# Performance work log

Measured on AMD Instinct MI355X. Metric: run time of the kernel, lower is better.

## Reference

```python
import jax, jax.numpy as jnp
import numpy as np

DIM = 512
NUM_HEADS = 8
HEAD_DIM = DIM // NUM_HEADS
SCALE = HEAD_DIM ** -0.5
HIDDEN = int(DIM * 4.0)
LN_EPS = 1e-5


def layer_norm(x, w, b):
    mu = jnp.mean(x, axis=-1, keepdims=True)
    var = jnp.var(x, axis=-1, keepdims=True)
    return (x - mu) * jax.lax.rsqrt(var + LN_EPS) * w + b


def setup_inputs() -> dict:
    key = jax.random.key(0)
    ks = jax.random.split(key, 8)
    s = 0.02
    return {
        "x": jax.random.normal(ks[0], (8, 4096, DIM), dtype=jnp.float32),
        "ln1_w": jnp.ones((DIM,), jnp.float32),
        "ln1_b": jnp.zeros((DIM,), jnp.float32),
        "qkv_w": jax.random.normal(ks[1], (3 * DIM, DIM), jnp.float32) * s,
        "proj_w": jax.random.normal(ks[2], (DIM, DIM), jnp.float32) * s,
        "proj_b": jnp.zeros((DIM,), jnp.float32),
        "ln2_w": jnp.ones((DIM,), jnp.float32),
        "ln2_b": jnp.zeros((DIM,), jnp.float32),
        "fc1_w": jax.random.normal(ks[3], (HIDDEN, DIM), jnp.float32) * s,
        "fc1_b": jnp.zeros((HIDDEN,), jnp.float32),
        "fc2_w": jax.random.normal(ks[4], (DIM, HIDDEN), jnp.float32) * s,
        "fc2_b": jnp.zeros((DIM,), jnp.float32),
        "eca_w": jax.random.normal(ks[5], (1, 1, 3), jnp.float32) * 0.5,
    }


def channel_attention(x, qkv_w, proj_w, proj_b):
    B, N, C = x.shape
    qkv = (x @ qkv_w.T).reshape(B, N, 3, NUM_HEADS, HEAD_DIM)
    qkv = qkv.transpose(2, 0, 3, 1, 4)  # (3, B, h, N, hd)
    q, k, v = qkv[0], qkv[1] * SCALE, qkv[2]
    # cross-covariance attention: (hd x hd) per head
    attn = jax.nn.softmax(jnp.einsum("bhnd,bhne->bhde", k, v), axis=-1)
    out = jnp.einsum("bhde,bhne->bhnd", attn, q)  # (B, h, N, hd)
    out = out.transpose(0, 2, 1, 3).reshape(B, N, C)
    return out @ proj_w.T + proj_b


def mlp_eca(x, fc1_w, fc1_b, fc2_w, fc2_b, eca_w):
    B, N, C = x.shape
    H = W = int(np.sqrt(N))
    h = jax.nn.gelu(x @ fc1_w.T + fc1_b, approximate=False)
    y = h @ fc2_w.T + fc2_b  # (B, N, C)
    # faithful replication of torch .view(B, C, H, W) on contiguous (B, N, C)
    y4 = y.reshape(B, C, H, W)
    pooled = jnp.mean(y4, axis=(2, 3))  # (B, C)
    conv = jax.lax.conv_general_dilated(
        pooled[:, None, :], eca_w, window_strides=(1,), padding=[(1, 1)],
        dimension_numbers=("NCW", "OIW", "NCW"))[:, 0, :]  # (B, C)
    gate = jax.nn.sigmoid(conv)[:, :, None, None]
    y4 = y4 * gate + y4
    return y4.reshape(B, C, H * W).transpose(0, 2, 1)  # (B, N, C)


def reference(x, ln1_w, ln1_b, qkv_w, proj_w, proj_b, ln2_w, ln2_b,
              fc1_w, fc1_b, fc2_w, fc2_b, eca_w):
    cur = layer_norm(x, ln1_w, ln1_b)
    x = x + channel_attention(cur, qkv_w, proj_w, proj_b)
    x = x + mlp_eca(layer_norm(x, ln2_w, ln2_b), fc1_w, fc1_b, fc2_w, fc2_b, eca_w)
    return x
```

## Files before the change

### kernel.cpp

```cpp
#include <hip/hip_runtime.h>
#include <hip/hip_bf16.h>

typedef __bf16 bf16;
typedef __bf16 bf16x8 __attribute__((ext_vector_type(8)));
typedef float floatx4 __attribute__((ext_vector_type(4)));

#define B_    8
#define N_    4096
#define C_    512
#define BN_   32768
#define HID_  2048
#define SCALE_ 0.125f

__device__ __forceinline__ void load_lds16(const void* g, void* l) {
    __builtin_amdgcn_global_load_lds(
        (const __attribute__((address_space(1))) void*)g,
        (__attribute__((address_space(3))) void*)l, 16, 0, 0);
}

__device__ __forceinline__ float gelu_fast(float v) {
    float c = fmaf(v * v, 0.044715f, 1.0f) * v;
    float e = __builtin_amdgcn_exp2f(-2.3022082f * c);
    return v * __builtin_amdgcn_rcpf(1.0f + e);
}

__global__ void sniff_kernel(const unsigned int* __restrict__ xw, int* __restrict__ flag)
{
    int t = threadIdx.x;
    int votes = 0;
#pragma unroll
    for (int i = 0; i < 4; i++) {
        unsigned w = xw[t * 4 + i];
        if (w == 0u) continue;
        unsigned a = w & 0xFFFFu;
        unsigned e = (a >> 7) & 0xFFu;
        if (a != 0u && e >= 110u && e <= 135u) votes++; else votes--;
    }
#pragma unroll
    for (int off = 32; off; off >>= 1) votes += __shfl_xor(votes, off);
    __shared__ int s[4];
    if ((t & 63) == 0) s[t >> 6] = votes;
    __syncthreads();
    if (t == 0) *flag = (s[0] + s[1] + s[2] + s[3]) > 0 ? 1 : 0;
}

struct ConvArgs {
    const void* src[12];
    unsigned    dstoff[12];
    int         n[12];
};

__global__ __launch_bounds__(256) void convert_params(
    ConvArgs args, char* __restrict__ ws, const int* __restrict__ flag)
{
    int seg = blockIdx.y;
    int n = args.n[seg];
    int base = blockIdx.x * 2048;
    if (base >= n) return;
    bf16* dst = (bf16*)(ws + args.dstoff[seg]);
    const void* src = args.src[seg];
    bool isbf = (*flag != 0);
#pragma unroll
    for (int j = 0; j < 8; j++) {
        int idx = base + threadIdx.x + j * 256;
        if (idx < n) {
            float v = isbf ? (float)((const bf16*)src)[idx]
                           : ((const float*)src)[idx];
            dst[idx] = (bf16)v;
        }
    }
}

__device__ __forceinline__ void ln_core(float f[8], const bf16* w, const bf16* b,
                                        int lane, bf16* outp)
{
    float s = 0.f, sq = 0.f;
#pragma unroll
    for (int j = 0; j < 8; j++) { s += f[j]; sq += f[j]*f[j]; }
#pragma unroll
    for (int off = 32; off; off >>= 1) { s += __shfl_xor(s, off); sq += __shfl_xor(sq, off); }
    float mean = s * (1.f/512.f);
    float var  = sq * (1.f/512.f) - mean*mean;
    float inv  = rsqrtf(var + 1e-5f);
    bf16x8 wv = *(const bf16x8*)(w + lane*8);
    bf16x8 bv = *(const bf16x8*)(b + lane*8);
    bf16x8 o;
#pragma unroll
    for (int j = 0; j < 8; j++) o[j] = (bf16)((f[j]-mean)*inv*(float)wv[j] + (float)bv[j]);
    *(bf16x8*)outp = o;
}

__global__ __launch_bounds__(256) void ln_dyn_kernel(
    const void* __restrict__ xv, const bf16* __restrict__ w,
    const bf16* __restrict__ b, bf16* __restrict__ out, const int* __restrict__ flag)
{
    int wave = threadIdx.x >> 6, lane = threadIdx.x & 63;
    size_t row = (size_t)blockIdx.x * 4 + wave;
    float f[8];
    if (*flag) {
        bf16x8 v = *(const bf16x8*)((const bf16*)xv + row * C_ + lane * 8);
#pragma unroll
        for (int j = 0; j < 8; j++) f[j] = (float)v[j];
    } else {
        const float4* p = (const float4*)((const float*)xv + row * C_ + lane * 8);
        float4 v0 = p[0], v1 = p[1];
        f[0]=v0.x; f[1]=v0.y; f[2]=v0.z; f[3]=v0.w;
        f[4]=v1.x; f[5]=v1.y; f[6]=v1.z; f[7]=v1.w;
    }
    ln_core(f, w, b, lane, out + row * C_ + lane*8);
}

__global__ __launch_bounds__(256) void ln_b16_kernel(
    const bf16* __restrict__ x, const bf16* __restrict__ w,
    const bf16* __restrict__ b, bf16* __restrict__ out)
{
    int wave = threadIdx.x >> 6, lane = threadIdx.x & 63;
    size_t row = (size_t)blockIdx.x * 4 + wave;
    bf16x8 v = *(const bf16x8*)(x + row * C_ + lane * 8);
    float f[8];
#pragma unroll
    for (int j = 0; j < 8; j++) f[j] = (float)v[j];
    ln_core(f, w, b, lane, out + row * C_ + lane*8);
}

__global__ __launch_bounds__(256) void ln_f32_kernel(
    const float* __restrict__ x, const bf16* __restrict__ w,
    const bf16* __restrict__ b, bf16* __restrict__ out)
{
    int wave = threadIdx.x >> 6, lane = threadIdx.x & 63;
    size_t row = (size_t)blockIdx.x * 4 + wave;
    const float4* p = (const float4*)(x + row * C_ + lane * 8);
    float4 v0 = p[0], v1 = p[1];
    float f[8] = { v0.x, v0.y, v0.z, v0.w, v1.x, v1.y, v1.z, v1.w };
    ln_core(f, w, b, lane, out + row * C_ + lane*8);
}

enum { EPI_NONE = 0, EPI_BIAS = 1, EPI_BIAS_RESID = 2, EPI_BIAS_GELU = 3, EPI_QKV = 4 };

#define RD_A(dst, S, H)                                                        \
    _Pragma("unroll") for (int mi = 0; mi < 4; mi++) {                         \
        int row = wm * 64 + mi * 16 + l16;                                     \
        _Pragma("unroll") for (int ks = 0; ks < 2; ks++)                       \
            dst[mi][ks] = *(const bf16x8*)(&Asl[S][H][0][0] + row * 64 +       \
                ((ks * 32 + quad * 8) ^ ((row & 7) << 3)));                    \
    }
#define RD_B(dst, S, H)                                                        \
    _Pragma("unroll") for (int ni = 0; ni < 2; ni++) {                         \
        int row = wn * 32 + ni * 16 + l16;                                     \
        _Pragma("unroll") for (int ks = 0; ks < 2; ks++)                       \
            dst[ni][ks] = *(const bf16x8*)(&Bsl[S][H][0][0] + row * 64 +       \
                ((ks * 32 + quad * 8) ^ ((row & 7) << 3)));                    \
    }
#define MM(AF, BF, AH, BH)                                                     \
    __builtin_amdgcn_s_setprio(1);                                             \
    _Pragma("unroll") for (int mi = 0; mi < 4; mi++)                           \
    _Pragma("unroll") for (int ni = 0; ni < 2; ni++)                           \
    _Pragma("unroll") for (int ks = 0; ks < 2; ks++)                           \
        acc[(AH)*4+mi][(BH)*2+ni] = __builtin_amdgcn_mfma_f32_16x16x32_bf16(   \
            AF[mi][ks], BF[ni][ks], acc[(AH)*4+mi][(BH)*2+ni], 0, 0, 0);       \
    __builtin_amdgcn_s_setprio(0);
#define STAGE2(GB, LB)                                                         \
    { load_lds16((GB) + goff0, (LB) + loff0);                                  \
      load_lds16((GB) + goff1, (LB) + loff1); }

template<typename OutT, int EPI>
__global__ __launch_bounds__(512, 2) void gemm256(
    const bf16* __restrict__ A, const bf16* __restrict__ W,
    const bf16* __restrict__ bias, const void* __restrict__ resid,
    const int* __restrict__ flag,
    OutT* __restrict__ Cout, bf16* __restrict__ Cout2, int M, int Nn, int K)
{
    __shared__ bf16 Asl[2][2][128][64];
    __shared__ bf16 Bsl[2][2][128][64];
    const int t = threadIdx.x;
    const int wv = t >> 6, lane = t & 63;
    const int quad = lane >> 4, l16 = lane & 15;
    const int wm = wv >> 2, wn = wv & 3;
    const int Nt = Nn >> 8;
    const int total = (M >> 8) * Nt;
    const int G = gridDim.x;
    const int NKT = K >> 6;

    const int c0 = t, c1 = 512 + t;
    const int r0 = c0 >> 3, r1 = c1 >> 3;
    const size_t goff0 = (size_t)r0 * K + (size_t)(((c0 & 7) ^ (r0 & 7)) * 8);
    const size_t goff1 = (size_t)r1 * K + (size_t)(((c1 & 7) ^ (r1 & 7)) * 8);
    const int loff0 = c0 * 8, loff1 = c1 * 8;

    int id = blockIdx.x;
    if (id >= total) return;
    int m0 = (((id >> 3) / Nt) * 8 + (id & 7)) * 256;
    int n0 = ((id >> 3) % Nt) * 256;

    STAGE2(A + (size_t)m0 * K,         &Asl[0][0][0][0]);
    STAGE2(W + (size_t)n0 * K,         &Bsl[0][0][0][0]);
    STAGE2(A + (size_t)(m0 + 128) * K, &Asl[0][1][0][0]);
    STAGE2(W + (size_t)n0 * K + 64,    &Bsl[1][0][0][0]);
    STAGE2(W + (size_t)(n0 + 128) * K, &Bsl[0][1][0][0]);
    STAGE2(A + (size_t)m0 * K + 64,    &Asl[1][0][0][0]);
    asm volatile("s_waitcnt vmcnt(4)");
    __builtin_amdgcn_s_barrier();

    bf16x8 afE[4][2], afO[4][2], bf0[2][2], bf1[2][2];
    RD_A(afE, 0, 0)

    for (;;) {
        const int idn = id + G;
        const bool hn = idn < total;
        int m0n = 0, n0n = 0;
        if (hn) {
            m0n = (((idn >> 3) / Nt) * 8 + (idn & 7)) * 256;
            n0n = ((idn >> 3) % Nt) * 256;
        }

        floatx4 acc[8][4] = {};

        for (int kt = 0; kt < NKT; ++kt) {
            const int s = kt & 1;
            {
                const bf16* p = (kt + 1 < NKT)
                    ? A + (size_t)(m0 + 128) * K + (size_t)(kt + 1) * 64
                    : (hn ? A + (size_t)(m0n + 128) * K : nullptr);
                if (p) STAGE2(p, &Asl[s ^ 1][1][0][0]);
            }
            __builtin_amdgcn_s_barrier();
            RD_B(bf0, s, 0)
            RD_B(bf1, s, 1)
            __builtin_amdgcn_sched_barrier(0);
            MM(afE, bf0, 0, 0)
            {
                const bf16* p = (kt + 1 < NKT)
                    ? W + (size_t)(n0 + 128) * K + (size_t)(kt + 1) * 64
                    : (hn ? W + (size_t)(n0n + 128) * K : nullptr);
                if (p) STAGE2(p, &Bsl[s ^ 1][1][0][0]);
            }
            __builtin_amdgcn_s_barrier();
            RD_A(afO, s, 1)
            __builtin_amdgcn_sched_barrier(0);
            MM(afE, bf1, 0, 1)
            {
                const bf16* p = (kt + 2 < NKT)
                    ? A + (size_t)m0 * K + (size_t)(kt + 2) * 64
                    : (hn ? A + (size_t)m0n * K + (size_t)(kt + 2 - NKT) * 64 : nullptr);
                if (p) STAGE2(p, &Asl[s][0][0][0]);
            }
            __builtin_amdgcn_s_barrier();
            MM(afO, bf1, 1, 1)
            {
                const bf16* p = (kt + 2 < NKT)
                    ? W + (size_t)n0 * K + (size_t)(kt + 2) * 64
                    : (hn ? W + (size_t)n0n * K + (size_t)(kt + 2 - NKT) * 64 : nullptr);
                if (p) STAGE2(p, &Bsl[s][0][0][0]);
            }
            if (kt + 1 < NKT || hn) {
                if (kt + 2 < NKT || hn) asm volatile("s_waitcnt vmcnt(4)");
                else                    asm volatile("s_waitcnt vmcnt(0)");
            }
            __builtin_amdgcn_s_barrier();
            if (kt + 1 < NKT || hn) { RD_A(afE, s ^ 1, 0) }
            __builtin_amdgcn_sched_barrier(0);
            MM(afO, bf0, 1, 0)
        }

        size_t ldc = (size_t)Nn; int csub = 0; bool to2 = false;
        if (EPI == EPI_QKV) {
            if (n0 >= 512) { to2 = true; ldc = 1024; csub = 512; }
            else           { ldc = 512; }
        }
        bool isbf = false;
        if (EPI == EPI_BIAS_RESID) isbf = (*flag != 0);

#pragma unroll
        for (int mg = 0; mg < 8; mg++) {
            int rowg = m0 + (mg >> 2) * 128 + wm * 64 + (mg & 3) * 16 + quad * 4;
#pragma unroll
            for (int ng = 0; ng < 4; ng++) {
                int col = n0 + (ng >> 1) * 128 + wn * 32 + (ng & 1) * 16 + l16;
                float bv = (EPI == EPI_BIAS || EPI == EPI_BIAS_RESID || EPI == EPI_BIAS_GELU)
                           ? (float)bias[col] : 0.f;
#pragma unroll
                for (int r = 0; r < 4; r++) {
                    size_t idx = (size_t)(rowg + r) * ldc + (col - csub);
                    float v = acc[mg][ng][r] + bv;
                    if (EPI == EPI_BIAS_RESID) {
                        float rres = isbf ? (float)((const bf16*)resid)[idx]
                                          : ((const float*)resid)[idx];
                        v += rres;
                    }
                    if (EPI == EPI_BIAS_GELU)  v = gelu_fast(v);
                    if (EPI == EPI_QKV && to2) Cout2[idx] = (bf16)v;
                    else                       Cout[idx]  = (OutT)v;
                }
            }
        }

        if (!hn) break;
        id = idn; m0 = m0n; n0 = n0n;
    }
}

__global__ __launch_bounds__(256) void attn_logits_mfma(
    const bf16* __restrict__ kv, float* __restrict__ partial)
{
    __shared__ bf16 Kt[64][136];
    __shared__ bf16 Vt[64][136];
    int s = blockIdx.x, bh = blockIdx.y, b = bh >> 3, h = bh & 7;
    int t = threadIdx.x, wave = t >> 6, lane = t & 63;
    int quad = lane >> 4, l16 = lane & 15;
    floatx4 acc[4] = {};
    for (int c = 0; c < 4; c++) {
        int n0 = s * 512 + c * 128;
        {
            int isv = t >> 7;
            int r   = t & 127;
            const bf16* gp = &kv[((size_t)b * N_ + n0 + r) * 1024 + h * 64 + isv * 512];
            bf16x8 rowv[8];
#pragma unroll
            for (int u = 0; u < 8; u++) rowv[u] = *(const bf16x8*)(gp + u * 8);
            bf16 (*dst)[136] = isv ? Vt : Kt;
#pragma unroll
            for (int u = 0; u < 8; u++)
#pragma unroll
                for (int jj = 0; jj < 8; jj++)
                    dst[u * 8 + jj][r] = rowv[u][jj];
        }
        __syncthreads();
#pragma unroll
        for (int ks = 0; ks < 4; ks++) {
            bf16x8 af = *(const bf16x8*)&Kt[wave * 16 + l16][ks * 32 + quad * 8];
#pragma unroll
            for (int ni = 0; ni < 4; ni++) {
                bf16x8 bfv = *(const bf16x8*)&Vt[ni * 16 + l16][ks * 32 + quad * 8];
                acc[ni] = __builtin_amdgcn_mfma_f32_16x16x32_bf16(af, bfv, acc[ni], 0, 0, 0);
            }
        }
        __syncthreads();
    }
    float* p = partial + ((size_t)bh * 8 + s) * 4096;
#pragma unroll
    for (int ni = 0; ni < 4; ni++)
#pragma unroll
        for (int r = 0; r < 4; r++)
            p[(wave * 16 + quad * 4 + r) * 64 + ni * 16 + l16] = acc[ni][r];
}

__global__ __launch_bounds__(256) void attn_softmax_kernel(
    const float* __restrict__ partial, bf16* __restrict__ attnb)
{
    int bh = blockIdx.y;
    int wave = threadIdx.x >> 6, lane = threadIdx.x & 63;
    for (int r = 0; r < 4; r++) {
        int d = blockIdx.x * 16 + wave * 4 + r;
        float v = 0.f;
#pragma unroll
        for (int s = 0; s < 8; s++) v += partial[((size_t)bh*8 + s)*4096 + d*64 + lane];
        v *= SCALE_;
        float m = v;
#pragma unroll
        for (int off = 32; off; off >>= 1) m = fmaxf(m, __shfl_xor(m, off));
        float p = expf(v - m);
        float sum = p;
#pragma unroll
        for (int off = 32; off; off >>= 1) sum += __shfl_xor(sum, off);
        attnb[(size_t)bh*4096 + d*64 + lane] = (bf16)(p / sum);
    }
}

__global__ __launch_bounds__(256) void attn_apply_mfma(
    const bf16* __restrict__ q, const bf16* __restrict__ attnb,
    bf16* __restrict__ outT)
{
    int bh = blockIdx.y, b = bh >> 3, h = bh & 7;
    int t = threadIdx.x, wave = t >> 6, lane = t & 63;
    int quad = lane >> 4, l16 = lane & 15;
    int nbase = blockIdx.x * 256 + wave * 64;
    bf16x8 bfrag[4][2];
#pragma unroll
    for (int di = 0; di < 4; di++)
#pragma unroll
        for (int ks = 0; ks < 2; ks++)
            bfrag[di][ks] = *(const bf16x8*)&attnb[(size_t)bh*4096 + (di*16 + l16)*64 + ks*32 + quad*8];
    floatx4 acc[4][4] = {};
#pragma unroll
    for (int mi = 0; mi < 4; mi++) {
#pragma unroll
        for (int ks = 0; ks < 2; ks++) {
            bf16x8 af = *(const bf16x8*)&q[((size_t)b*N_ + nbase + mi*16 + l16)*512 + h*64 + ks*32 + quad*8];
#pragma unroll
            for (int di = 0; di < 4; di++)
                acc[mi][di] = __builtin_amdgcn_mfma_f32_16x16x32_bf16(af, bfrag[di][ks], acc[mi][di], 0, 0, 0);
        }
    }
#pragma unroll
    for (int mi = 0; mi < 4; mi++)
#pragma unroll
        for (int di = 0; di < 4; di++)
#pragma unroll
            for (int r = 0; r < 4; r++)
                outT[((size_t)b*N_ + nbase + mi*16 + quad*4 + r)*512 + h*64 + di*16 + l16] =
                    (bf16)acc[mi][di][r];
}

__global__ __launch_bounds__(256) void pooled_kernel(
    const bf16* __restrict__ y, float* __restrict__ pooled)
{
    int bc = blockIdx.x;
    const bf16* p = y + (size_t)bc * 4096 + threadIdx.x * 16;
    float s = 0.f;
#pragma unroll
    for (int i = 0; i < 2; i++) {
        bf16x8 v = *(const bf16x8*)(p + i*8);
#pragma unroll
        for (int j = 0; j < 8; j++) s += (float)v[j];
    }
#pragma unroll
    for (int off = 32; off; off >>= 1) s += __shfl_xor(s, off);
    __shared__ float red[4];
    if ((threadIdx.x & 63) == 0) red[threadIdx.x >> 6] = s;
    __syncthreads();
    if (threadIdx.x == 0)
        pooled[bc] = (red[0] + red[1] + red[2] + red[3]) * (1.f/4096.f);
}

__global__ void gate_kernel(const float* __restrict__ pooled,
                            const bf16* __restrict__ eca_w, float* __restrict__ gate1)
{
    int c = threadIdx.x, b = blockIdx.x;
    float w0 = (float)eca_w[0], w1 = (float)eca_w[1], w2 = (float)eca_w[2];
    const float* p = pooled + b * 512;
    float conv = w1 * p[c];
    if (c > 0)   conv += w0 * p[c-1];
    if (c < 511) conv += w2 * p[c+1];
    float g = 1.f / (1.f + expf(-conv));
    gate1[b * 512 + c] = 1.f + g;
}

__global__ __launch_bounds__(256) void final_rmw(
    const bf16* __restrict__ y, const float* __restrict__ gate1,
    float* __restrict__ out)
{
    int b = blockIdx.z, c0 = blockIdx.y * 64, n0 = blockIdx.x * 64;
    __shared__ float ytile[64][65];
    int t = threadIdx.x;
#pragma unroll
    for (int i = 0; i < 2; i++) {
        int chunk = t * 2 + i;
        int ci = chunk >> 3, nj = (chunk & 7) * 8;
        bf16x8 v = *(const bf16x8*)&y[(size_t)b * ((size_t)N_*C_) + (size_t)(c0+ci) * 4096 + n0 + nj];
#pragma unroll
        for (int j = 0; j < 8; j++) ytile[ci][nj+j] = (float)v[j];
    }
    __syncthreads();
    int cc = t & 63, nb = t >> 6;
    float g = gate1[b * 512 + c0 + cc];
    for (int p = 0; p < 16; p++) {
        int nr = p * 4 + nb;
        size_t idx = ((size_t)b * N_ + n0 + nr) * C_ + c0 + cc;
        out[idx] = out[idx] + g * ytile[cc][nr];
    }
}

__global__ __launch_bounds__(256) void final_fresh(
    const bf16* __restrict__ y, const bf16* __restrict__ x2b,
    const float* __restrict__ gate1, float* __restrict__ out)
{
    int b = blockIdx.z, c0 = blockIdx.y * 64, n0 = blockIdx.x * 64;
    __shared__ float ytile[64][65];
    int t = threadIdx.x;
#pragma unroll
    for (int i = 0; i < 2; i++) {
        int chunk = t * 2 + i;
        int ci = chunk >> 3, nj = (chunk & 7) * 8;
        bf16x8 v = *(const bf16x8*)&y[(size_t)b * ((size_t)N_*C_) + (size_t)(c0+ci) * 4096 + n0 + nj];
#pragma unroll
        for (int j = 0; j < 8; j++) ytile[ci][nj+j] = (float)v[j];
    }
    __syncthreads();
    int cc = t & 63, nb = t >> 6;
    float g = gate1[b * 512 + c0 + cc];
    for (int p = 0; p < 16; p++) {
        int nr = p * 4 + nb;
        size_t idx = ((size_t)b * N_ + n0 + nr) * C_ + c0 + cc;
        out[idx] = (float)x2b[idx] + g * ytile[cc][nr];
    }
}

extern "C" void kernel_launch(void* const* d_in, const int* in_sizes, int n_in,
                              void* d_out, int out_size, void* d_ws, size_t ws_size,
                              hipStream_t stream)
{
    float* outf = (float*)d_out;
    bf16*  outb = (bf16*)d_out;
    char* ws = (char*)d_ws;

    int*   flag    = (int*)ws;
    float* pooled  = (float*)(ws + 4096);
    float* gate1   = (float*)(ws + 20480);
    bf16* ln1_w = (bf16*)(ws + 65536);
    bf16* ln1_b = (bf16*)(ws + 67584);
    bf16* ln2_w = (bf16*)(ws + 69632);
    bf16* ln2_b = (bf16*)(ws + 71680);
    bf16* proj_b= (bf16*)(ws + 73728);
    bf16* fc2_b = (bf16*)(ws + 75776);
    bf16* eca_w = (bf16*)(ws + 77824);
    bf16* fc1_b = (bf16*)(ws + 81920);
    bf16* qkv_w = (bf16*)(ws + ((size_t)1 << 20));
    bf16* proj_w= (bf16*)(ws + (size_t)2621440);
    bf16* fc1_w = (bf16*)(ws + ((size_t)3 << 20));
    bf16* fc2_w = (bf16*)(ws + ((size_t)5 << 20));
    float* partial = (float*)(ws + ((size_t)7  << 20));
    bf16*  attnb   = (bf16*)(ws + ((size_t)15 << 20));
    bf16*  T1      = (bf16*)(ws + ((size_t)16 << 20));
    bf16*  kvbuf   = (bf16*)(ws + ((size_t)48 << 20));
    bf16*  hbuf    = kvbuf;
    bf16*  x2b     = (bf16*)(ws + ((size_t)176 << 20));

    const bool fat = ws_size >= ((size_t)212 << 20);

    sniff_kernel<<<1, 256, 0, stream>>>((const unsigned int*)d_in[0], flag);

    ConvArgs ca;
    const int   srcidx[12] = { 1, 2, 6, 7, 5, 11, 12, 9, 3, 4, 8, 10 };
    const unsigned offs[12] = { 65536, 67584, 69632, 71680, 73728, 75776, 77824, 81920,
                                1u<<20, 2621440u, 3u<<20, 5u<<20 };
    for (int i = 0; i < 12; i++) {
        ca.src[i] = d_in[srcidx[i]];
        ca.dstoff[i] = offs[i];
        ca.n[i] = in_sizes[srcidx[i]];
    }
    convert_params<<<dim3(512, 12), 256, 0, stream>>>(ca, ws, flag);

    ln_dyn_kernel<<<BN_/4, 256, 0, stream>>>(d_in[0], ln1_w, ln1_b, T1, flag);

    gemm256<bf16, EPI_QKV><<<256, 512, 0, stream>>>(
        T1, qkv_w, nullptr, nullptr, flag, outb, kvbuf, BN_, 1536, 512);

    attn_logits_mfma<<<dim3(8, 64), 256, 0, stream>>>(kvbuf, partial);
    attn_softmax_kernel<<<dim3(4, 64), 256, 0, stream>>>(partial, attnb);
    attn_apply_mfma<<<dim3(16, 64), 256, 0, stream>>>(outb, attnb, T1);

    if (fat) {
        gemm256<bf16, EPI_BIAS_RESID><<<256, 512, 0, stream>>>(
            T1, proj_w, proj_b, d_in[0], flag, x2b, nullptr, BN_, 512, 512);
        ln_b16_kernel<<<BN_/4, 256, 0, stream>>>(x2b, ln2_w, ln2_b, T1);
        gemm256<bf16, EPI_BIAS_GELU><<<256, 512, 0, stream>>>(
            T1, fc1_w, fc1_b, nullptr, flag, hbuf, nullptr, BN_, 2048, 512);
        gemm256<bf16, EPI_BIAS><<<256, 512, 0, stream>>>(
            hbuf, fc2_w, fc2_b, nullptr, flag, T1, nullptr, BN_, 512, 2048);
        pooled_kernel<<<4096, 256, 0, stream>>>(T1, pooled);
        gate_kernel<<<8, 512, 0, stream>>>(pooled, eca_w, gate1);
        final_fresh<<<dim3(64, 8, 8), 256, 0, stream>>>(T1, x2b, gate1, outf);
    } else {
        gemm256<float, EPI_BIAS_RESID><<<256, 512, 0, stream>>>(
            T1, proj_w, proj_b, d_in[0], flag, outf, nullptr, BN_, 512, 512);
        ln_f32_kernel<<<BN_/4, 256, 0, stream>>>(outf, ln2_w, ln2_b, T1);
        for (int ch = 0; ch < 2; ch++) {
            bf16* Tch = T1 + (size_t)ch * 16384 * 512;
            gemm256<bf16, EPI_BIAS_GELU><<<256, 512, 0, stream>>>(
                Tch, fc1_w, fc1_b, nullptr, flag, hbuf, nullptr, 16384, 2048, 512);
            gemm256<bf16, EPI_BIAS><<<128, 512, 0, stream>>>(
                hbuf, fc2_w, fc2_b, nullptr, flag, Tch, nullptr, 16384, 512, 2048);
        }
        pooled_kernel<<<4096, 256, 0, stream>>>(T1, pooled);
        gate_kernel<<<8, 512, 0, stream>>>(pooled, eca_w, gate1);
        final_rmw<<<dim3(64, 8, 8), 256, 0, stream>>>(T1, gate1, outf);
    }
}
```

Baseline: 538.1 us.

## Unroll GEMM k-loop by two with precomputed LDS fragment pointers

Restructures the inner loop of the 256x256 bf16 GEMM into a two-stage unrolled KTILE macro, so the LDS double-buffer stage index is a compile-time constant. Swizzled LDS read addresses are precomputed once into pointer arrays instead of being recomputed on every read. The A-fragment prefetch across iterations is replaced by a single fragment buffer refilled inside each phase, with an explicit lgkmcnt(0) wait before each MFMA group. The prologue load order is also changed so the second half of the W tile is resident before the first barrier. This aims to cut address arithmetic and register pressure, but it gives up some overlap of LDS reads with MFMA work.

Result: faster. 521.9 us (-3.0%).

```diff
diff --git a/kernel.cpp b/kernel.cpp
--- a/kernel.cpp
+++ b/kernel.cpp
@@ -137,20 +137,6 @@
 
 enum { EPI_NONE = 0, EPI_BIAS = 1, EPI_BIAS_RESID = 2, EPI_BIAS_GELU = 3, EPI_QKV = 4 };
 
-#define RD_A(dst, S, H)                                                        \
-    _Pragma("unroll") for (int mi = 0; mi < 4; mi++) {                         \
-        int row = wm * 64 + mi * 16 + l16;                                     \
-        _Pragma("unroll") for (int ks = 0; ks < 2; ks++)                       \
-            dst[mi][ks] = *(const bf16x8*)(&Asl[S][H][0][0] + row * 64 +       \
-                ((ks * 32 + quad * 8) ^ ((row & 7) << 3)));                    \
-    }
-#define RD_B(dst, S, H)                                                        \
-    _Pragma("unroll") for (int ni = 0; ni < 2; ni++) {                         \
-        int row = wn * 32 + ni * 16 + l16;                                     \
-        _Pragma("unroll") for (int ks = 0; ks < 2; ks++)                       \
-            dst[ni][ks] = *(const bf16x8*)(&Bsl[S][H][0][0] + row * 64 +       \
-                ((ks * 32 + quad * 8) ^ ((row & 7) << 3)));                    \
-    }
 #define MM(AF, BF, AH, BH)                                                     \
     __builtin_amdgcn_s_setprio(1);                                             \
     _Pragma("unroll") for (int mi = 0; mi < 4; mi++)                           \
@@ -163,6 +149,63 @@
     { load_lds16((GB) + goff0, (LB) + loff0);                                  \
       load_lds16((GB) + goff1, (LB) + loff1); }
 
+#define KTILE(KT, S)                                                           \
+{                                                                              \
+    bf16x8 af[4][2], bf0[2][2], bf1[2][2];                                     \
+                         \
+    _Pragma("unroll") for (int mi = 0; mi < 4; mi++)                           \
+    _Pragma("unroll") for (int ks = 0; ks < 2; ks++)                           \
+        af[mi][ks] = *(const bf16x8*)(pa[mi][ks] + (S) * 16384);               \
+    _Pragma("unroll") for (int ni = 0; ni < 2; ni++)                           \
+    _Pragma("unroll") for (int ks = 0; ks < 2; ks++)                           \
+        bf0[ni][ks] = *(const bf16x8*)(pb[ni][ks] + (S) * 16384);              \
+    { const bf16* sp = ((KT) + 1 < NKT)                                        \
+          ? A + (size_t)(m0 + 128) * K + (size_t)((KT) + 1) * 64               \
+          : (hn ? A + (size_t)(m0n + 128) * K : nullptr);                      \
+      if (sp) STAGE2(sp, &Asl[(S) ^ 1][1][0][0]); }                            \
+    __builtin_amdgcn_s_barrier();                                              \
+    asm volatile("s_waitcnt lgkmcnt(0)");                                      \
+    __builtin_amdgcn_sched_barrier(0);                                         \
+    MM(af, bf0, 0, 0)                                                          \
+                             \
+    _Pragma("unroll") for (int ni = 0; ni < 2; ni++)                           \
+    _Pragma("unroll") for (int ks = 0; ks < 2; ks++)                           \
+        bf1[ni][ks] = *(const bf16x8*)(pb[ni][ks] + (S) * 16384 + 8192);       \
+    { const bf16* sp = ((KT) + 1 < NKT)                                        \
+          ? W + (size_t)(n0 + 128) * K + (size_t)((KT) + 1) * 64               \
+          : (hn ? W + (size_t)(n0n + 128) * K : nullptr);                      \
+      if (sp) STAGE2(sp, &Bsl[(S) ^ 1][1][0][0]); }                            \
+    __builtin_amdgcn_s_barrier();                                              \
+    asm volatile("s_waitcnt lgkmcnt(0)");                                      \
+    __builtin_amdgcn_sched_barrier(0);                                         \
+    MM(af, bf1, 0, 1)                                                          \
+                            \
+    _Pragma("unroll") for (int mi = 0; mi < 4; mi++)                           \
+    _Pragma("unroll") for (int ks = 0; ks < 2; ks++)                           \
+        af[mi][ks] = *(const bf16x8*)(pa[mi][ks] + (S) * 16384 + 8192);        \
+    { const bf16* sp = ((KT) + 2 < NKT)                                        \
+          ? A + (size_t)m0 * K + (size_t)((KT) + 2) * 64                       \
+          : (hn ? A + (size_t)m0n * K + (size_t)((KT) + 2 - NKT) * 64          \
+               : nullptr);                                                     \
+      if (sp) STAGE2(sp, &Asl[(S)][0][0][0]); }                                \
+    __builtin_amdgcn_s_barrier();                                              \
+    asm volatile("s_waitcnt lgkmcnt(0)");                                      \
+    __builtin_amdgcn_sched_barrier(0);                                         \
+    MM(af, bf1, 1, 1)                                                          \
+               \
+    { const bf16* sp = ((KT) + 2 < NKT)                                        \
+          ? W + (size_t)n0 * K + (size_t)((KT) + 2) * 64                       \
+          : (hn ? W + (size_t)n0n * K + (size_t)((KT) + 2 - NKT) * 64          \
+               : nullptr);                                                     \
+      if (sp) STAGE2(sp, &Bsl[(S)][0][0][0]); }                                \
+    if ((KT) + 1 < NKT || hn) {                                                \
+        if ((KT) + 2 < NKT || hn) asm volatile("s_waitcnt vmcnt(4)");          \
+        else                      asm volatile("s_waitcnt vmcnt(0)");          \
+    }                                                                          \
+    __builtin_amdgcn_s_barrier();                                              \
+    MM(af, bf0, 1, 0)                                                          \
+}
+
 template<typename OutT, int EPI>
 __global__ __launch_bounds__(512, 2) void gemm256(
     const bf16* __restrict__ A, const bf16* __restrict__ W,
@@ -181,6 +224,25 @@
     const int G = gridDim.x;
     const int NKT = K >> 6;
 
+    const bf16* pa[4][2];
+    const bf16* pb[2][2];
+#pragma unroll
+    for (int mi = 0; mi < 4; mi++) {
+        int row = wm * 64 + mi * 16 + l16;
+#pragma unroll
+        for (int ks = 0; ks < 2; ks++)
+            pa[mi][ks] = &Asl[0][0][0][0] + row * 64 +
+                         ((ks * 32 + quad * 8) ^ ((row & 7) << 3));
+    }
+#pragma unroll
+    for (int ni = 0; ni < 2; ni++) {
+        int row = wn * 32 + ni * 16 + l16;
+#pragma unroll
+        for (int ks = 0; ks < 2; ks++)
+            pb[ni][ks] = &Bsl[0][0][0][0] + row * 64 +
+                         ((ks * 32 + quad * 8) ^ ((row & 7) << 3));
+    }
+
     const int c0 = t, c1 = 512 + t;
     const int r0 = c0 >> 3, r1 = c1 >> 3;
     const size_t goff0 = (size_t)r0 * K + (size_t)(((c0 & 7) ^ (r0 & 7)) * 8);
@@ -195,14 +257,11 @@
     STAGE2(A + (size_t)m0 * K,         &Asl[0][0][0][0]);
     STAGE2(W + (size_t)n0 * K,         &Bsl[0][0][0][0]);
     STAGE2(A + (size_t)(m0 + 128) * K, &Asl[0][1][0][0]);
-    STAGE2(W + (size_t)n0 * K + 64,    &Bsl[1][0][0][0]);
     STAGE2(W + (size_t)(n0 + 128) * K, &Bsl[0][1][0][0]);
     STAGE2(A + (size_t)m0 * K + 64,    &Asl[1][0][0][0]);
+    STAGE2(W + (size_t)n0 * K + 64,    &Bsl[1][0][0][0]);
     asm volatile("s_waitcnt vmcnt(4)");
     __builtin_amdgcn_s_barrier();
-
-    bf16x8 afE[4][2], afO[4][2], bf0[2][2], bf1[2][2];
-    RD_A(afE, 0, 0)
 
     for (;;) {
         const int idn = id + G;
@@ -215,51 +274,9 @@
 
         floatx4 acc[8][4] = {};
 
-        for (int kt = 0; kt < NKT; ++kt) {
-            const int s = kt & 1;
-            {
-                const bf16* p = (kt + 1 < NKT)
-                    ? A + (size_t)(m0 + 128) * K + (size_t)(kt + 1) * 64
-                    : (hn ? A + (size_t)(m0n + 128) * K : nullptr);
-                if (p) STAGE2(p, &Asl[s ^ 1][1][0][0]);
-            }
-            __builtin_amdgcn_s_barrier();
-            RD_B(bf0, s, 0)
-            RD_B(bf1, s, 1)
-            __builtin_amdgcn_sched_barrier(0);
-            MM(afE, bf0, 0, 0)
-            {
-                const bf16* p = (kt + 1 < NKT)
-                    ? W + (size_t)(n0 + 128) * K + (size_t)(kt + 1) * 64
-                    : (hn ? W + (size_t)(n0n + 128) * K : nullptr);
-                if (p) STAGE2(p, &Bsl[s ^ 1][1][0][0]);
-            }
-            __builtin_amdgcn_s_barrier();
-            RD_A(afO, s, 1)
-            __builtin_amdgcn_sched_barrier(0);
-            MM(afE, bf1, 0, 1)
-            {
-                const bf16* p = (kt + 2 < NKT)
-                    ? A + (size_t)m0 * K + (size_t)(kt + 2) * 64
-                    : (hn ? A + (size_t)m0n * K + (size_t)(kt + 2 - NKT) * 64 : nullptr);
-                if (p) STAGE2(p, &Asl[s][0][0][0]);
-            }
-            __builtin_amdgcn_s_barrier();
-            MM(afO, bf1, 1, 1)
-            {
-                const bf16* p = (kt + 2 < NKT)
-                    ? W + (size_t)n0 * K + (size_t)(kt + 2) * 64
-                    : (hn ? W + (size_t)n0n * K + (size_t)(kt + 2 - NKT) * 64 : nullptr);
-                if (p) STAGE2(p, &Bsl[s][0][0][0]);
-            }
-            if (kt + 1 < NKT || hn) {
-                if (kt + 2 < NKT || hn) asm volatile("s_waitcnt vmcnt(4)");
-                else                    asm volatile("s_waitcnt vmcnt(0)");
-            }
-            __builtin_amdgcn_s_barrier();
-            if (kt + 1 < NKT || hn) { RD_A(afE, s ^ 1, 0) }
-            __builtin_amdgcn_sched_barrier(0);
-            MM(afO, bf0, 1, 0)
+        for (int kt = 0; kt < NKT; kt += 2) {
+            KTILE(kt, 0)
+            KTILE(kt + 1, 1)
         }
 
         size_t ldc = (size_t)Nn; int csub = 0; bool to2 = false;
```
